# Optimization experiments

Hardware: AMD Instinct MI355X
Metric: run time of the kernel (lower is better)

The kernel has to match this reference:

```python
import jax, jax.numpy as jnp
import numpy as np

N = 32768        # tokens (batch*seq)
D = 1024         # input_dim
E = 64           # n_experts
TOPK = 2


def setup_inputs() -> dict:
    key = jax.random.key(0)
    k_x, k_w, k_b, k_wn, k_bn = jax.random.split(key, 5)
    scale = 1.0 / np.sqrt(D)
    return {
        "x": jax.random.normal(k_x, (N, D), dtype=jnp.float32),
        "W": jax.random.uniform(k_w, (D, E), minval=-scale, maxval=scale, dtype=jnp.float32),
        "b": jax.random.uniform(k_b, (E,), minval=-scale, maxval=scale, dtype=jnp.float32),
        "W_noise": jax.random.uniform(k_wn, (D, E), minval=-scale, maxval=scale, dtype=jnp.float32),
        "b_noise": jax.random.uniform(k_bn, (E,), minval=-scale, maxval=scale, dtype=jnp.float32),
    }


def reference(x, W, b, W_noise, b_noise):
    # logits = fc(x): single Linear (router_hidden_dims=[])
    logits = x @ W + b                      # [N, E]
    # training=False (default): no noise path; fc_noise params unused
    topk_logits, topk_indices = jax.lax.top_k(logits, TOPK)  # [N, k]
    # scatter topk logits into a -inf tensor, then softmax
    mask = jnp.sum(jax.nn.one_hot(topk_indices, E, dtype=jnp.bool_), axis=-2)  # [N, E]
    sparse_logits = jnp.where(mask, logits, -jnp.inf)
    routing_probs = jax.nn.softmax(sparse_logits, axis=-1)  # zeros off-topk
    return routing_probs, topk_indices
```

## Files before the change

kernel.cpp:

```cpp
#include <hip/hip_runtime.h>
#include <cstdint>
#include <cstddef>

#define N_TOK 32768
#define DIM   1024
#define NE    64
#define RPB   64
#define KHALF 512
#define CHUNK 32
#define NCHUNK (KHALF / CHUNK)

__device__ __forceinline__ void gload16(const float* g, float* l) {
  __builtin_amdgcn_global_load_lds(
      (const __attribute__((address_space(1))) uint32_t*)g,
      (__attribute__((address_space(3))) uint32_t*)l, 16, 0, 0);
}

__global__ __launch_bounds__(512, 4) void router_kernel(
    const float* __restrict__ x, const float* __restrict__ W,
    const float* __restrict__ bias, float* __restrict__ probs,
    float* __restrict__ idxo) {
  __shared__ __align__(1024) float xs[2][2][RPB][CHUNK];
  __shared__ float  red[4][RPB][16];
  __shared__ float4 ex[4][RPB];
  __shared__ float4 ex2[RPB];

  const int tid  = threadIdx.x;
  const int lane = tid & 63;
  const int w    = __builtin_amdgcn_readfirstlane(tid >> 6);
  const int g    = w & 3;
  const int h    = w >> 2;
  const int r0   = blockIdx.x * RPB;

  auto stage = [&](int cc) {
    const int buf = cc & 1;
    float* base = &xs[h][buf][0][0];
    const int k0 = h * KHALF + cc * CHUNK;
#pragma unroll
    for (int jj = 0; jj < 2; ++jj) {
      const int j = 2 * g + jj;
      const int row = 8 * j + (lane >> 3);
      const int sq  = (lane & 7) ^ (lane >> 3);
      gload16(x + (size_t)(r0 + row) * DIM + k0 + (sq << 2),
              base + j * 256);
    }
  };

  float acc[16];
#pragma unroll
  for (int e = 0; e < 16; ++e) acc[e] = 0.0f;

  stage(0);

  for (int cc = 0; cc < NCHUNK; ++cc) {
    __syncthreads();
    if (cc + 1 < NCHUNK) stage(cc + 1);

    const int buf = cc & 1;
    const float* xb = &xs[h][buf][0][0] + lane * CHUNK;
    const float* Wc = W + (size_t)(h * KHALF + cc * CHUNK) * NE + g * 16;

    float4 xq = make_float4(0.f, 0.f, 0.f, 0.f);
#pragma unroll
    for (int kk = 0; kk < CHUNK; ++kk) {
      if ((kk & 3) == 0) {
        const int slot = (kk >> 2) ^ (lane & 7);
        xq = *(const float4*)(xb + (slot << 2));
      }
      const float xc = ((kk & 3) == 0) ? xq.x
                     : ((kk & 3) == 1) ? xq.y
                     : ((kk & 3) == 2) ? xq.z : xq.w;
      const float* Wk = Wc + (size_t)kk * NE;
#pragma unroll
      for (int e = 0; e < 16; ++e)
        acc[e] = fmaf(Wk[e], xc, acc[e]);
    }
  }

  __syncthreads();
  if (h == 1) {
#pragma unroll
    for (int q = 0; q < 4; ++q)
      *(float4*)&red[g][lane][q * 4] = make_float4(acc[q*4+0], acc[q*4+1],
                                                   acc[q*4+2], acc[q*4+3]);
  }
  __syncthreads();

  if (h == 0) {
#pragma unroll
    for (int q = 0; q < 4; ++q) {
      float4 r = *(const float4*)&red[g][lane][q * 4];
      acc[q*4+0] += r.x; acc[q*4+1] += r.y; acc[q*4+2] += r.z; acc[q*4+3] += r.w;
    }
#pragma unroll
    for (int e = 0; e < 16; ++e) acc[e] += bias[g * 16 + e];

    float v1, v2; int j1, j2;
    if (acc[1] > acc[0]) { v1 = acc[1]; j1 = 1; v2 = acc[0]; j2 = 0; }
    else                 { v1 = acc[0]; j1 = 0; v2 = acc[1]; j2 = 1; }
#pragma unroll
    for (int e = 2; e < 16; ++e) {
      if (acc[e] > v1)      { v2 = v1; j2 = j1; v1 = acc[e]; j1 = e; }
      else if (acc[e] > v2) { v2 = acc[e]; j2 = e; }
    }
    ex[g][lane] = make_float4(v1, v2, (float)(g * 16 + j1), (float)(g * 16 + j2));
  }
  __syncthreads();

  if (w == 0) {
    float4 m = ex[0][lane];
    float V1 = m.x, V2 = m.y, J1 = m.z, J2 = m.w;
#pragma unroll
    for (int gg = 1; gg < 4; ++gg) {
      float4 u = ex[gg][lane];
      if (u.x > V1) {
        bool s = (u.y > V1);
        V2 = s ? u.y : V1; J2 = s ? u.w : J1;
        V1 = u.x; J1 = u.z;
      } else if (u.x > V2) { V2 = u.x; J2 = u.z; }
    }
    const float e2 = __expf(V2 - V1);
    const float p1 = 1.0f / (1.0f + e2);
    const float p2 = e2 * p1;
    ex2[lane] = make_float4(J1, J2, p1, p2);
    float2 oi; oi.x = J1; oi.y = J2;
    *(float2*)(idxo + (size_t)(r0 + lane) * 2) = oi;
  }
  __syncthreads();

  if (h == 0) {
    float4 f = ex2[lane];
    const int ij1 = (int)f.x, ij2 = (int)f.y;
    float* op = probs + (size_t)(r0 + lane) * NE + g * 16;
#pragma unroll
    for (int q = 0; q < 4; ++q) {
      float4 o;
      const int e0 = g * 16 + q * 4;
      o.x = (e0 + 0 == ij1) ? f.z : (e0 + 0 == ij2) ? f.w : 0.0f;
      o.y = (e0 + 1 == ij1) ? f.z : (e0 + 1 == ij2) ? f.w : 0.0f;
      o.z = (e0 + 2 == ij1) ? f.z : (e0 + 2 == ij2) ? f.w : 0.0f;
      o.w = (e0 + 3 == ij1) ? f.z : (e0 + 3 == ij2) ? f.w : 0.0f;
      *(float4*)(op + q * 4) = o;
    }
  }
}

extern "C" void kernel_launch(void* const* d_in, const int* in_sizes, int n_in,
                              void* d_out, int out_size, void* d_ws, size_t ws_size,
                              hipStream_t stream) {
  (void)in_sizes; (void)n_in; (void)out_size; (void)d_ws; (void)ws_size;
  const float* x = (const float*)d_in[0];
  const float* W = (const float*)d_in[1];
  const float* b = (const float*)d_in[2];
  float* out  = (float*)d_out;
  float* idxo = out + (size_t)N_TOK * NE;

  dim3 grid(N_TOK / RPB);
  dim3 block(512);
  hipLaunchKernelGGL(router_kernel, grid, block, 0, stream, x, W, b, out, idxo);
}
```

Baseline: 248.6 us.

## Load x rows directly per lane, use scalar W loads, scatter probs

```diff
diff --git a/kernel.cpp b/kernel.cpp
--- a/kernel.cpp
+++ b/kernel.cpp
@@ -6,142 +6,107 @@
 #define DIM   1024
 #define NE    64
 #define RPB   64
-#define KHALF 512
-#define CHUNK 32
-#define NCHUNK (KHALF / CHUNK)
+#define KQ    256
+#define RSTR  36
 
-__device__ __forceinline__ void gload16(const float* g, float* l) {
-  __builtin_amdgcn_global_load_lds(
-      (const __attribute__((address_space(1))) uint32_t*)g,
-      (__attribute__((address_space(3))) uint32_t*)l, 16, 0, 0);
-}
+typedef __attribute__((ext_vector_type(16))) float f16v;
+typedef const __attribute__((address_space(4))) float*  cfp;
+typedef const __attribute__((address_space(4))) f16v*   cfp16;
 
 __global__ __launch_bounds__(512, 4) void router_kernel(
     const float* __restrict__ x, const float* __restrict__ W,
     const float* __restrict__ bias, float* __restrict__ probs,
     float* __restrict__ idxo) {
-  __shared__ __align__(1024) float xs[2][2][RPB][CHUNK];
-  __shared__ float  red[4][RPB][16];
-  __shared__ float4 ex[4][RPB];
-  __shared__ float4 ex2[RPB];
+  __shared__ float  red[2][3][RPB][RSTR];
+  __shared__ float4 mg[2][RPB];
 
   const int tid  = threadIdx.x;
   const int lane = tid & 63;
   const int w    = __builtin_amdgcn_readfirstlane(tid >> 6);
-  const int g    = w & 3;
-  const int h    = w >> 2;
+  const int eh   = w & 1;
+  const int kq   = w >> 1;
   const int r0   = blockIdx.x * RPB;
+  const int row  = r0 + lane;
 
-  auto stage = [&](int cc) {
-    const int buf = cc & 1;
-    float* base = &xs[h][buf][0][0];
-    const int k0 = h * KHALF + cc * CHUNK;
+  {
+    float4* pt = (float4*)(probs + (size_t)r0 * NE);
+    const float4 z = make_float4(0.f, 0.f, 0.f, 0.f);
+    pt[tid]       = z;
+    pt[tid + 512] = z;
+  }
+
+  float acc[32];
 #pragma unroll
-    for (int jj = 0; jj < 2; ++jj) {
-      const int j = 2 * g + jj;
-      const int row = 8 * j + (lane >> 3);
-      const int sq  = (lane & 7) ^ (lane >> 3);
-      gload16(x + (size_t)(r0 + row) * DIM + k0 + (sq << 2),
-              base + j * 256);
-    }
-  };
+  for (int e = 0; e < 32; ++e) acc[e] = 0.0f;
 
-  float acc[16];
+  const float* xr = x + (size_t)row * DIM + kq * KQ;
+  cfp WC = (cfp)(uintptr_t)(W + (size_t)kq * KQ * NE + eh * 32);
+
+  for (int k4 = 0; k4 < KQ / 4; ++k4) {
+    const float4 xv = *(const float4*)(xr + k4 * 4);
 #pragma unroll
-  for (int e = 0; e < 16; ++e) acc[e] = 0.0f;
-
-  stage(0);
-
-  for (int cc = 0; cc < NCHUNK; ++cc) {
-    __syncthreads();
-    if (cc + 1 < NCHUNK) stage(cc + 1);
-
-    const int buf = cc & 1;
-    const float* xb = &xs[h][buf][0][0] + lane * CHUNK;
-    const float* Wc = W + (size_t)(h * KHALF + cc * CHUNK) * NE + g * 16;
-
-    float4 xq = make_float4(0.f, 0.f, 0.f, 0.f);
+    for (int j = 0; j < 4; ++j) {
+      const int k = k4 * 4 + j;
+      const f16v wa = *(cfp16)(WC + (size_t)k * NE);
+      const f16v wb = *(cfp16)(WC + (size_t)k * NE + 16);
+      const float xc = (j == 0) ? xv.x : (j == 1) ? xv.y : (j == 2) ? xv.z : xv.w;
 #pragma unroll
-    for (int kk = 0; kk < CHUNK; ++kk) {
-      if ((kk & 3) == 0) {
-        const int slot = (kk >> 2) ^ (lane & 7);
-        xq = *(const float4*)(xb + (slot << 2));
-      }
-      const float xc = ((kk & 3) == 0) ? xq.x
-                     : ((kk & 3) == 1) ? xq.y
-                     : ((kk & 3) == 2) ? xq.z : xq.w;
-      const float* Wk = Wc + (size_t)kk * NE;
+      for (int e = 0; e < 16; ++e) acc[e]      = fmaf(wa[e], xc, acc[e]);
 #pragma unroll
-      for (int e = 0; e < 16; ++e)
-        acc[e] = fmaf(Wk[e], xc, acc[e]);
+      for (int e = 0; e < 16; ++e) acc[16 + e] = fmaf(wb[e], xc, acc[16 + e]);
     }
   }
 
   __syncthreads();
-  if (h == 1) {
+  if (kq > 0) {
 #pragma unroll
-    for (int q = 0; q < 4; ++q)
-      *(float4*)&red[g][lane][q * 4] = make_float4(acc[q*4+0], acc[q*4+1],
-                                                   acc[q*4+2], acc[q*4+3]);
+    for (int q = 0; q < 8; ++q)
+      *(float4*)&red[eh][kq - 1][lane][q * 4] =
+          make_float4(acc[q*4+0], acc[q*4+1], acc[q*4+2], acc[q*4+3]);
   }
   __syncthreads();
 
-  if (h == 0) {
+  if (kq == 0) {
 #pragma unroll
-    for (int q = 0; q < 4; ++q) {
-      float4 r = *(const float4*)&red[g][lane][q * 4];
-      acc[q*4+0] += r.x; acc[q*4+1] += r.y; acc[q*4+2] += r.z; acc[q*4+3] += r.w;
-    }
+    for (int t = 0; t < 3; ++t)
 #pragma unroll
-    for (int e = 0; e < 16; ++e) acc[e] += bias[g * 16 + e];
+      for (int q = 0; q < 8; ++q) {
+        float4 r = *(const float4*)&red[eh][t][lane][q * 4];
+        acc[q*4+0] += r.x; acc[q*4+1] += r.y; acc[q*4+2] += r.z; acc[q*4+3] += r.w;
+      }
+    cfp bC = (cfp)(uintptr_t)(bias + eh * 32);
+#pragma unroll
+    for (int e = 0; e < 32; ++e) acc[e] += bC[e];
 
     float v1, v2; int j1, j2;
     if (acc[1] > acc[0]) { v1 = acc[1]; j1 = 1; v2 = acc[0]; j2 = 0; }
     else                 { v1 = acc[0]; j1 = 0; v2 = acc[1]; j2 = 1; }
 #pragma unroll
-    for (int e = 2; e < 16; ++e) {
+    for (int e = 2; e < 32; ++e) {
       if (acc[e] > v1)      { v2 = v1; j2 = j1; v1 = acc[e]; j1 = e; }
       else if (acc[e] > v2) { v2 = acc[e]; j2 = e; }
     }
-    ex[g][lane] = make_float4(v1, v2, (float)(g * 16 + j1), (float)(g * 16 + j2));
+    mg[eh][lane] = make_float4(v1, v2, (float)(eh * 32 + j1), (float)(eh * 32 + j2));
   }
   __syncthreads();
 
   if (w == 0) {
-    float4 m = ex[0][lane];
-    float V1 = m.x, V2 = m.y, J1 = m.z, J2 = m.w;
-#pragma unroll
-    for (int gg = 1; gg < 4; ++gg) {
-      float4 u = ex[gg][lane];
-      if (u.x > V1) {
-        bool s = (u.y > V1);
-        V2 = s ? u.y : V1; J2 = s ? u.w : J1;
-        V1 = u.x; J1 = u.z;
-      } else if (u.x > V2) { V2 = u.x; J2 = u.z; }
-    }
+    const float4 a = mg[0][lane], b2 = mg[1][lane];
+    float V1 = a.x, V2 = a.y, J1 = a.z, J2 = a.w;
+    if (b2.x > V1) {
+      const bool s = (b2.y > V1);
+      V2 = s ? b2.y : V1; J2 = s ? b2.w : J1;
+      V1 = b2.x; J1 = b2.z;
+    } else if (b2.x > V2) { V2 = b2.x; J2 = b2.z; }
+
     const float e2 = __expf(V2 - V1);
     const float p1 = 1.0f / (1.0f + e2);
     const float p2 = e2 * p1;
-    ex2[lane] = make_float4(J1, J2, p1, p2);
-    float2 oi; oi.x = J1; oi.y = J2;
-    *(float2*)(idxo + (size_t)(r0 + lane) * 2) = oi;
-  }
-  __syncthreads();
 
-  if (h == 0) {
-    float4 f = ex2[lane];
-    const int ij1 = (int)f.x, ij2 = (int)f.y;
-    float* op = probs + (size_t)(r0 + lane) * NE + g * 16;
-#pragma unroll
-    for (int q = 0; q < 4; ++q) {
-      float4 o;
-      const int e0 = g * 16 + q * 4;
-      o.x = (e0 + 0 == ij1) ? f.z : (e0 + 0 == ij2) ? f.w : 0.0f;
-      o.y = (e0 + 1 == ij1) ? f.z : (e0 + 1 == ij2) ? f.w : 0.0f;
-      o.z = (e0 + 2 == ij1) ? f.z : (e0 + 2 == ij2) ? f.w : 0.0f;
-      o.w = (e0 + 3 == ij1) ? f.z : (e0 + 3 == ij2) ? f.w : 0.0f;
-      *(float4*)(op + q * 4) = o;
-    }
+    float* pr = probs + (size_t)row * NE;
+    pr[(int)J1] = p1;
+    pr[(int)J2] = p2;
+    *(float2*)(idxo + (size_t)row * 2) = make_float2(J1, J2);
   }
 }
 
```

Measured after the change: 251.5 us. No clear change (+1.2%).
